# Optimization experiments

Hardware: AMD Instinct MI355X
Metric: run time of the kernel (lower is better)

## Reference

```python
import jax, jax.numpy as jnp
import numpy as np

K = 20
EPS_BN = 1e-5

def knn_idx(x, k):
    # x: [B,N,C] -> k nearest neighbor indices [B,N,k] (self included, as in DGCNN)
    sq = jnp.sum(x * x, axis=-1)                       # [B,N]
    inner = jnp.einsum('bnc,bmc->bnm', x, x)           # [B,N,N]
    neg_dist = 2.0 * inner - sq[:, :, None] - sq[:, None, :]
    _, idx = jax.lax.top_k(neg_dist, k)
    return jax.lax.stop_gradient(idx)

def edge_feat(x, idx):
    # x: [B,N,C], idx: [B,N,k] -> [B,N,k,2C] = cat([x_j - x_i, x_i])
    nbr = jax.vmap(lambda xb, ib: xb[ib])(x, idx)      # [B,N,k,C]
    ctr = jnp.broadcast_to(x[:, :, None, :], nbr.shape)
    return jnp.concatenate([nbr - ctr, ctr], axis=-1)

def edge_conv(x, W, g, b, k):
    e = edge_feat(x, knn_idx(x, k))                    # dynamic kNN graph per layer
    h = jnp.einsum('bnkc,cd->bnkd', e, W)              # 1x1 conv2d
    h = h * (g / jnp.sqrt(1.0 + EPS_BN)) + b           # BN eval (mean=0, var=1)
    return jnp.max(jax.nn.leaky_relu(h, 0.2), axis=2)  # max over neighbors -> [B,N,d]

def layer_norm(x, g, b):
    m = jnp.mean(x, axis=-1, keepdims=True)
    v = jnp.var(x, axis=-1, keepdims=True)
    return (x - m) * jax.lax.rsqrt(v + 1e-5) * g + b

def setup_inputs():
    key = jax.random.key(0)
    B, N = 2, 4096
    ks = jax.random.split(key, 16)
    w = lambda i, shape: jax.random.normal(ks[i], shape, jnp.float32) * 0.05
    ones = lambda d: jnp.ones((d,), jnp.float32)
    zeros = lambda d: jnp.zeros((d,), jnp.float32)
    return dict(
        xyz=jax.random.normal(ks[0], (N, 3), jnp.float32),
        scale=jax.random.normal(ks[1], (N, 3), jnp.float32),
        rot=jax.random.normal(ks[2], (N, 4), jnp.float32),
        opacity=jax.random.normal(ks[3], (N, 1), jnp.float32),
        color=jax.random.normal(ks[4], (N, 3), jnp.float32),
        pose=jax.random.normal(ks[5], (B, 75), jnp.float32),
        lbs_weights=jax.random.normal(ks[6], (N, 24), jnp.float32),
        Wc1=w(7, (226, 64)), g1=ones(64), b1=zeros(64),
        Wc2=w(8, (128, 64)), g2=ones(64), b2=zeros(64),
        Wc3=w(9, (128, 128)), g3=ones(128), b3=zeros(128),
        Wc4=w(10, (256, 256)), g4=ones(256), b4=zeros(256),
        Wc5=w(11, (512, 128)), g5=ones(128), b5=zeros(128),
        Wo1=w(12, (128, 128)), bo1=zeros(128), lg1=ones(128), lb1=zeros(128),
        Wo2=w(13, (128, 128)), bo2=zeros(128), lg2=ones(128), lb2=zeros(128),
        Wo3=w(14, (128, 38)), bo3=zeros(38),
    )

def reference(xyz, scale, rot, opacity, color, pose, lbs_weights,
              Wc1, g1, b1, Wc2, g2, b2, Wc3, g3, b3, Wc4, g4, b4, Wc5, g5, b5,
              Wo1, bo1, lg1, lb1, Wo2, bo2, lg2, lb2, Wo3, bo3):
    B, N = pose.shape[0], xyz.shape[0]
    gfeat = jnp.concatenate([xyz, scale, rot, opacity, color], axis=-1)   # [N,14]
    feats = jnp.concatenate([
        jnp.broadcast_to(gfeat[None], (B, N, gfeat.shape[-1])),
        jnp.broadcast_to(lbs_weights[None], (B, N, lbs_weights.shape[-1])),
        jnp.broadcast_to(pose[:, None, :], (B, N, pose.shape[-1])),
    ], axis=-1)                                                            # [B,N,113]
    # DGCNN graph encoder (dynamic kNN EdgeConv stack)
    x1 = edge_conv(feats, Wc1, g1, b1, K)   # [B,N,64]
    x2 = edge_conv(x1, Wc2, g2, b2, K)      # [B,N,64]
    x3 = edge_conv(x2, Wc3, g3, b3, K)      # [B,N,128]
    x4 = edge_conv(x3, Wc4, g4, b4, K)      # [B,N,256]
    cat = jnp.concatenate([x1, x2, x3, x4], axis=-1)                      # [B,N,512]
    gf = jax.nn.leaky_relu(
        jnp.einsum('bnc,cd->bnd', cat, Wc5) * (g5 / jnp.sqrt(1.0 + EPS_BN)) + b5, 0.2)
    # offset predictor MLP
    h = jax.nn.leaky_relu(layer_norm(gf @ Wo1 + bo1, lg1, lb1), 0.2)
    h = jax.nn.leaky_relu(layer_norm(h @ Wo2 + bo2, lg2, lb2), 0.2)
    off = h @ Wo3 + bo3                                                   # [B,N,38]
    # residual add of gaussian offsets (first 14 dims), lbs offsets raw (last 24)
    out = jnp.concatenate([gfeat[None] + off[..., :14], off[..., 14:]], axis=-1)
    return out                                                            # [B,N,38]
```

## Files before the change

kernel.cpp:

```cpp
#include <hip/hip_runtime.h>
#include <math.h>

#define KNN 20
#define BN_INV 0.9999950000374997f

__device__ __forceinline__ unsigned f2o(float f){
    unsigned u = __float_as_uint(f);
    return (u >> 31) ? ~u : (u | 0x80000000u);
}
__device__ __forceinline__ float o2f(unsigned u){
    return __uint_as_float((u >> 31) ? (u & 0x7fffffffu) : ~u);
}
__device__ __forceinline__ float leaky(float v){ return v > 0.f ? v : 0.2f * v; }

__global__ __launch_bounds__(128) void build_feats_kernel(
    const float* __restrict__ xyz, const float* __restrict__ scale,
    const float* __restrict__ rot, const float* __restrict__ opac,
    const float* __restrict__ color, const float* __restrict__ pose,
    const float* __restrict__ lbs, float* __restrict__ feats,
    float* __restrict__ sqout, int N)
{
    __shared__ float sred[2];
    int row = blockIdx.x;
    int b = row / N, n = row % N;
    int c = threadIdx.x;
    float v = 0.f;
    if      (c <   3) v = xyz  [n*3 + c];
    else if (c <   6) v = scale[n*3 + c-3];
    else if (c <  10) v = rot  [n*4 + c-6];
    else if (c <  11) v = opac [n];
    else if (c <  14) v = color[n*3 + c-11];
    else if (c <  38) v = lbs  [n*24 + c-14];
    else if (c < 113) v = pose [b*75 + c-38];
    if (c < 116) feats[(long)row*116 + c] = v;
    float ss = v * v;
    #pragma unroll
    for (int off = 32; off; off >>= 1) ss += __shfl_xor(ss, off);
    if ((c & 63) == 0) sred[c >> 6] = ss;
    __syncthreads();
    if (c == 0) sqout[row] = sred[0] + sred[1];
}


template<int C>
__global__ __launch_bounds__(256) void dist_gemm_kernel(
    const float* __restrict__ x, int N, int CP, float* __restrict__ G)
{
    __shared__ __align__(16) float smem[2*128*68];
    float (*xi)[68] = (float(*)[68])smem;
    float (*xj)[68] = (float(*)[68])(smem + 128*68);

    if (blockIdx.y < blockIdx.x) return;
    const int b  = blockIdx.z;
    const int bi = blockIdx.x * 128;
    const int bj = blockIdx.y * 128;
    const int t  = threadIdx.x;
    const int tx = t & 15, ty = t >> 4;
    const int CP4 = CP / 4;
    const long base = (long)b * N;
    const float4* xp = (const float4*)x;

    float acc[8][8] = {};

    for (int c0 = 0; c0 < C; c0 += 64){
        const int KCc = (C - c0 < 64) ? (C - c0) : 64;
        const int KC4 = KCc >> 2;
        __syncthreads();
        for (int f = t; f < 128 * KC4; f += 256){
            int r = f / KC4, c4 = f - r * KC4;
            float4 a = xp[(base + bi + r) * CP4 + (c0 >> 2) + c4];
            float4 bv = xp[(base + bj + r) * CP4 + (c0 >> 2) + c4];
            *(float4*)&xi[r][c4 * 4] = a;
            *(float4*)&xj[r][c4 * 4] = bv;
        }
        __syncthreads();
        for (int c = 0; c < KCc; c += 4){
            float4 A[8], Bv[8];
            #pragma unroll
            for (int ii = 0; ii < 8; ++ii) A[ii]  = *(const float4*)&xi[ty + 16*ii][c];
            #pragma unroll
            for (int jj = 0; jj < 8; ++jj) Bv[jj] = *(const float4*)&xj[tx + 16*jj][c];
            #pragma unroll
            for (int ii = 0; ii < 8; ++ii)
                #pragma unroll
                for (int jj = 0; jj < 8; ++jj){
                    acc[ii][jj] = fmaf(A[ii].x, Bv[jj].x, acc[ii][jj]);
                    acc[ii][jj] = fmaf(A[ii].y, Bv[jj].y, acc[ii][jj]);
                    acc[ii][jj] = fmaf(A[ii].z, Bv[jj].z, acc[ii][jj]);
                    acc[ii][jj] = fmaf(A[ii].w, Bv[jj].w, acc[ii][jj]);
                }
        }
    }

    #pragma unroll
    for (int ii = 0; ii < 8; ++ii){
        long rbase = (base + bi + ty + 16*ii) * N + bj;
        #pragma unroll
        for (int jj = 0; jj < 8; ++jj)
            G[rbase + tx + 16*jj] = acc[ii][jj];
    }

    if (bi != bj){
        __syncthreads();
        float (*tr)[132] = (float(*)[132])smem;
        #pragma unroll
        for (int ii = 0; ii < 8; ++ii)
            #pragma unroll
            for (int jj = 0; jj < 8; ++jj)
                tr[tx + 16*jj][ty + 16*ii] = acc[ii][jj];
        __syncthreads();
        const int r0 = t >> 5;
        const int cc = (t & 31) * 4;
        #pragma unroll
        for (int f = 0; f < 16; ++f){
            int r = r0 + 8 * f;
            *(float4*)&G[(base + bj + r) * N + bi + cc] = *(const float4*)&tr[r][cc];
        }
    }
}

#define TCAP 256
__global__ __launch_bounds__(256) void topk_kernel(
    const float* __restrict__ G, const float* __restrict__ sq,
    int N, int* __restrict__ idx_out)
{
    __shared__ unsigned smax[256];
    __shared__ unsigned cand_u[TCAP];
    __shared__ int      cand_j[TCAP];
    __shared__ unsigned cand_cnt;
    __shared__ unsigned sTu;

    const int row = blockIdx.x;
    const int b   = row >> 12;
    const int t   = threadIdx.x;
    const float4* g4  = (const float4*)(G  + (long)row * 4096);
    const float4* sq4 = (const float4*)(sq + (long)b   * 4096);

    unsigned u[16];
    #pragma unroll
    for (int qq = 0; qq < 4; ++qq){
        int v4 = t + 256 * qq;
        float4 gg = g4[v4];
        float4 ss = sq4[v4];
        u[4*qq+0] = f2o(fmaf(2.f, gg.x, -ss.x));
        u[4*qq+1] = f2o(fmaf(2.f, gg.y, -ss.y));
        u[4*qq+2] = f2o(fmaf(2.f, gg.z, -ss.z));
        u[4*qq+3] = f2o(fmaf(2.f, gg.w, -ss.w));
    }

    unsigned mu = u[0];
    #pragma unroll
    for (int q = 1; q < 16; ++q) mu = u[q] > mu ? u[q] : mu;
    smax[t] = mu;
    if (t == 0) cand_cnt = 0;
    __syncthreads();

    int rank = 0;
    for (int k = 0; k < 256; ++k){
        unsigned ou = smax[k];
        rank += (ou > mu) || (ou == mu && k < t);
    }
    if (rank == KNN - 1) sTu = mu;
    __syncthreads();
    const unsigned Tu = sTu;

    #pragma unroll
    for (int qq = 0; qq < 4; ++qq)
        #pragma unroll
        for (int m = 0; m < 4; ++m){
            int q = 4*qq + m;
            if (u[q] >= Tu){
                unsigned p = atomicAdd(&cand_cnt, 1u);
                if (p < TCAP){ cand_u[p] = u[q]; cand_j[p] = 4*(t + 256*qq) + m; }
            }
        }
    __syncthreads();
    const int cc = (int)cand_cnt;

    if (cc <= TCAP){
        if (t < cc){
            unsigned cu = cand_u[t]; int cj = cand_j[t];
            int r = 0;
            for (int k = 0; k < cc; ++k){
                unsigned ou = cand_u[k];
                r += (ou > cu) || (ou == cu && cand_j[k] < cj);
            }
            if (r < KNN) idx_out[(long)row * KNN + r] = cj;
        }
    } else {
        __shared__ unsigned rv[4]; __shared__ int ri[4]; __shared__ int gj_;
        unsigned lv = 0u; int lj = 0x7fffffff;
        #pragma unroll
        for (int q = 0; q < 16; ++q)
            if (u[q] > lv){ lv = u[q]; lj = 4*(t + 256*(q>>2)) + (q&3); }
        for (int it = 0; it < KNN; ++it){
            unsigned bv = lv; int bj = lj;
            #pragma unroll
            for (int off = 32; off; off >>= 1){
                unsigned ov = __shfl_xor(bv, off);
                int      oj = __shfl_xor(bj, off);
                if (ov > bv || (ov == bv && oj < bj)){ bv = ov; bj = oj; }
            }
            if ((t & 63) == 0){ rv[t >> 6] = bv; ri[t >> 6] = bj; }
            __syncthreads();
            if (t == 0){
                unsigned fv = rv[0]; int fj = ri[0];
                #pragma unroll
                for (int w = 1; w < 4; ++w)
                    if (rv[w] > fv || (rv[w] == fv && ri[w] < fj)){ fv = rv[w]; fj = ri[w]; }
                gj_ = fj;
                idx_out[(long)row * KNN + it] = fj;
            }
            __syncthreads();
            int fj = gj_;
            if (fj >= 0 && ((fj >> 2) & 255) == t){
                u[((fj >> 10) << 2) | (fj & 3)] = 0u;
                lv = 0u; lj = 0x7fffffff;
                #pragma unroll
                for (int q = 0; q < 16; ++q)
                    if (u[q] > lv){ lv = u[q]; lj = 4*(t + 256*(q>>2)) + (q&3); }
            }
            __syncthreads();
        }
    }
}


__global__ void prep_wcat_kernel(const float* __restrict__ W, int C, int CP, int D,
                                 float* __restrict__ Wcat)
{
    int i = blockIdx.x * 256 + threadIdx.x;
    int TWOD = 2 * D;
    if (i >= CP * TWOD) return;
    int c = i / TWOD, n = i - c * TWOD;
    float v = 0.f;
    if (c < C) v = (n < D) ? W[c*D + n] : (W[(C + c)*D + (n - D)] - W[c*D + (n - D)]);
    Wcat[i] = v;
}

__global__ __launch_bounds__(256) void gemm_pq_kernel(
    const float* __restrict__ X, int CP, const float* __restrict__ Wcat,
    const float* __restrict__ g, const float* __restrict__ bias,
    int D, int TWOD, float* __restrict__ PQ)
{
    __shared__ __align__(16) float As[128][68];
    __shared__ __align__(16) float Bs[64][132];
    const int bi = blockIdx.x * 128;
    const int bn = blockIdx.y * 128;
    const int t  = threadIdx.x;
    const int tx = t & 15, ty = t >> 4;
    const int CP4 = CP / 4;
    const float4* xp = (const float4*)X;

    float acc[8][8] = {};

    for (int c0 = 0; c0 < CP; c0 += 64){
        const int KC = (CP - c0 < 64) ? (CP - c0) : 64;
        const int KC4 = KC >> 2;
        __syncthreads();
        for (int f = t; f < 128 * KC4; f += 256){
            int r = f / KC4, c4 = f - r * KC4;
            *(float4*)&As[r][c4 * 4] = xp[(long)(bi + r) * CP4 + (c0 >> 2) + c4];
        }
        for (int f = t; f < KC * 32; f += 256){
            int r = f >> 5, c4 = f & 31;
            *(float4*)&Bs[r][c4 * 4] = *(const float4*)&Wcat[(long)(c0 + r) * TWOD + bn + c4 * 4];
        }
        __syncthreads();
        for (int c = 0; c < KC; c += 4){
            float4 A[8];
            #pragma unroll
            for (int ii = 0; ii < 8; ++ii) A[ii] = *(const float4*)&As[ty + 16*ii][c];
            float Bv0[8], Bv1[8], Bv2[8], Bv3[8];
            #pragma unroll
            for (int jj = 0; jj < 8; ++jj){
                Bv0[jj] = Bs[c+0][tx + 16*jj];
                Bv1[jj] = Bs[c+1][tx + 16*jj];
                Bv2[jj] = Bs[c+2][tx + 16*jj];
                Bv3[jj] = Bs[c+3][tx + 16*jj];
            }
            #pragma unroll
            for (int ii = 0; ii < 8; ++ii)
                #pragma unroll
                for (int jj = 0; jj < 8; ++jj){
                    acc[ii][jj] = fmaf(A[ii].x, Bv0[jj], acc[ii][jj]);
                    acc[ii][jj] = fmaf(A[ii].y, Bv1[jj], acc[ii][jj]);
                    acc[ii][jj] = fmaf(A[ii].z, Bv2[jj], acc[ii][jj]);
                    acc[ii][jj] = fmaf(A[ii].w, Bv3[jj], acc[ii][jj]);
                }
        }
    }

    #pragma unroll
    for (int jj = 0; jj < 8; ++jj){
        int n = bn + tx + 16*jj;
        int d = (n < D) ? n : n - D;
        float gg = g[d] * BN_INV;
        float bb = (n < D) ? 0.f : bias[d];
        #pragma unroll
        for (int ii = 0; ii < 8; ++ii)
            PQ[(long)(bi + ty + 16*ii) * TWOD + n] = fmaf(acc[ii][jj], gg, bb);
    }
}

template<int D, int RPB>
__global__ __launch_bounds__(256) void gather_max_kernel(
    const float* __restrict__ PQ, const int* __restrict__ idx, int N,
    float* __restrict__ y, float* __restrict__ sqout)
{
    __shared__ int   lidx[RPB][KNN];
    __shared__ float sred[4];
    const int rb = blockIdx.x * RPB;
    const int t  = threadIdx.x;
    if (t < RPB * KNN) lidx[t / KNN][t % KNN] = idx[(long)rb * KNN + t];
    __syncthreads();

    const int r = t / D, d = t - r * D;
    const int row = rb + r;
    const long base = (long)(row / N) * N;
    const int TWOD = 2 * D;

    float q = PQ[(long)row * TWOD + D + d];
    float m = -INFINITY;
    #pragma unroll
    for (int k = 0; k < KNN; ++k){
        int j = lidx[r][k];
        m = fmaxf(m, PQ[(base + j) * TWOD + d]);
    }
    float val = leaky(m + q);
    y[(long)row * D + d] = val;

    float ss = val * val;
    #pragma unroll
    for (int off = 32; off; off >>= 1) ss += __shfl_xor(ss, off);
    if ((t & 63) == 0) sred[t >> 6] = ss;
    __syncthreads();
    if (d == 0){
        constexpr int WPR = D / 64;
        float s = 0.f;
        int w0 = (r * D) >> 6;
        #pragma unroll
        for (int w = 0; w < WPR; ++w) s += sred[w0 + w];
        sqout[row] = s;
    }
}

__global__ __launch_bounds__(256) void knn_kernel(
    const float* __restrict__ x, int N, int CP4, int* __restrict__ idx_out)
{
    __shared__ float4 xi4[32];
    __shared__ float drow[4096];
    __shared__ float rv[4];
    __shared__ int   ri[4];

    int row = blockIdx.x;
    int b = row / N;
    int t = threadIdx.x;
    const float4* xp = (const float4*)x;

    if (t < CP4) xi4[t] = xp[(long)row * CP4 + t];
    __syncthreads();

    long bb = (long)b * N * CP4;
    for (int j = t; j < N; j += 256){
        const float4* p = xp + bb + (long)j * CP4;
        float acc = 0.f;
        #pragma unroll 4
        for (int c = 0; c < CP4; ++c){
            float4 xv = p[c], yv = xi4[c];
            float dx = xv.x - yv.x, dy = xv.y - yv.y;
            float dz = xv.z - yv.z, dw = xv.w - yv.w;
            acc += dx*dx + dy*dy + dz*dz + dw*dw;
        }
        drow[j] = -acc;
    }
    __syncthreads();

    for (int it = 0; it < KNN; ++it){
        float bv = -INFINITY; int bi = N;
        for (int j = t; j < N; j += 256){
            float v = drow[j];
            if (v > bv){ bv = v; bi = j; }
        }
        #pragma unroll
        for (int off = 32; off > 0; off >>= 1){
            float ov = __shfl_xor(bv, off);
            int   oi = __shfl_xor(bi, off);
            if (ov > bv || (ov == bv && oi < bi)){ bv = ov; bi = oi; }
        }
        if ((t & 63) == 0){ rv[t >> 6] = bv; ri[t >> 6] = bi; }
        __syncthreads();
        if (t == 0){
            float fv = rv[0]; int fi = ri[0];
            #pragma unroll
            for (int w = 1; w < 4; ++w){
                if (rv[w] > fv || (rv[w] == fv && ri[w] < fi)){ fv = rv[w]; fi = ri[w]; }
            }
            idx_out[(long)row * KNN + it] = fi;
            drow[fi] = -INFINITY;
        }
        __syncthreads();
    }
}

template<int D, int KPT>
__global__ __launch_bounds__(256) void edge_conv_kernel(
    const float* __restrict__ x, int N, int C, int CP,
    const float* __restrict__ W, const float* __restrict__ g,
    const float* __restrict__ bias, const int* __restrict__ idx,
    float* __restrict__ y, float* __restrict__ sqout)
{
    __shared__ float xi[128];
    __shared__ float nbr[KNN * 128];
    __shared__ float t2[D];
    __shared__ unsigned um[D];
    __shared__ float sred[4];

    int row = blockIdx.x;
    int b = row / N;
    int t = threadIdx.x;

    for (int c = t; c < C; c += 256) xi[c] = x[(long)row * CP + c];
    for (int kk = 0; kk < KNN; ++kk){
        int j = idx[(long)row * KNN + kk];
        long nb = ((long)b * N + j) * CP;
        for (int c = t; c < C; c += 256) nbr[kk * C + c] = x[nb + c];
    }
    __syncthreads();

    for (int d = t; d < D; d += 256){
        float s = 0.f;
        for (int c = 0; c < C; ++c) s += xi[c] * W[(C + c) * D + d];
        t2[d] = s; um[d] = 0u;
    }
    __syncthreads();

    const int d  = t % D;
    const int kg = t / D;
    float s[KPT];
    #pragma unroll
    for (int q = 0; q < KPT; ++q) s[q] = t2[d];

    const float* nb0 = &nbr[(kg * KPT) * C];
    for (int c = 0; c < C; ++c){
        float w   = W[c * D + d];
        float xic = xi[c];
        #pragma unroll
        for (int q = 0; q < KPT; ++q)
            s[q] += (nb0[q * C + c] - xic) * w;
    }
    float g_ = g[d] * BN_INV, b_ = bias[d];
    float m = -INFINITY;
    #pragma unroll
    for (int q = 0; q < KPT; ++q)
        m = fmaxf(m, leaky(s[q] * g_ + b_));
    atomicMax(&um[d], f2o(m));
    __syncthreads();

    float ss = 0.f;
    for (int dd = t; dd < D; dd += 256){
        float val = o2f(um[dd]);
        y[(long)row * D + dd] = val;
        ss += val * val;
    }
    #pragma unroll
    for (int off = 32; off; off >>= 1) ss += __shfl_xor(ss, off);
    if ((t & 63) == 0) sred[t >> 6] = ss;
    __syncthreads();
    if (t == 0) sqout[row] = sred[0] + sred[1] + sred[2] + sred[3];
}

#define HP 8
__global__ __launch_bounds__(128) void head_kernel(
    const float* __restrict__ x1, const float* __restrict__ x2,
    const float* __restrict__ x3, const float* __restrict__ x4,
    const float* __restrict__ feats,
    const float* __restrict__ Wc5, const float* __restrict__ g5, const float* __restrict__ b5,
    const float* __restrict__ Wo1, const float* __restrict__ bo1,
    const float* __restrict__ lg1, const float* __restrict__ lb1,
    const float* __restrict__ Wo2, const float* __restrict__ bo2,
    const float* __restrict__ lg2, const float* __restrict__ lb2,
    const float* __restrict__ Wo3, const float* __restrict__ bo3,
    float* __restrict__ out, int N, int R)
{
    __shared__ __align__(16) float cat[HP][520];
    __shared__ __align__(16) float hb[HP][132];
    __shared__ float wsum[2][HP], wsq[2][HP];
    __shared__ float f14[HP][14];

    const int t = threadIdx.x;
    const long p0 = (long)blockIdx.x * HP;
    const int wid = t >> 6;

    long rows[HP];
    #pragma unroll
    for (int p = 0; p < HP; ++p){
        long row = p0 + p; if (row >= R) row = R - 1;
        rows[p] = row;
        cat[p][t]       = (t < 64) ? x1[row*64 + t] : x2[row*64 + (t-64)];
        cat[p][128 + t] = x3[row*128 + t];
        cat[p][256 + t] = x4[row*256 + t];
        cat[p][384 + t] = x4[row*256 + 128 + t];
        if (t < 14) f14[p][t] = feats[row*116 + t];
    }
    __syncthreads();

    const float g5t = g5[t] * BN_INV, b5t = b5[t];
    float acc[HP];
    #pragma unroll
    for (int p = 0; p < HP; ++p) acc[p] = 0.f;
    for (int c4 = 0; c4 < 128; ++c4){
        float w0 = Wc5[(4*c4+0)*128 + t];
        float w1 = Wc5[(4*c4+1)*128 + t];
        float w2 = Wc5[(4*c4+2)*128 + t];
        float w3 = Wc5[(4*c4+3)*128 + t];
        #pragma unroll
        for (int p = 0; p < HP; ++p){
            float4 cv = *(const float4*)&cat[p][4*c4];
            acc[p] = fmaf(cv.x, w0, acc[p]);
            acc[p] = fmaf(cv.y, w1, acc[p]);
            acc[p] = fmaf(cv.z, w2, acc[p]);
            acc[p] = fmaf(cv.w, w3, acc[p]);
        }
    }
    #pragma unroll
    for (int p = 0; p < HP; ++p) hb[p][t] = leaky(fmaf(acc[p], g5t, b5t));
    __syncthreads();

    for (int layer = 0; layer < 2; ++layer){
        const float* W  = layer ? Wo2 : Wo1;
        const float* bo = layer ? bo2 : bo1;
        const float* lg = layer ? lg2 : lg1;
        const float* lb = layer ? lb2 : lb1;
        float a2[HP];
        float bot = bo[t];
        #pragma unroll
        for (int p = 0; p < HP; ++p) a2[p] = bot;
        for (int c4 = 0; c4 < 32; ++c4){
            float w0 = W[(4*c4+0)*128 + t];
            float w1 = W[(4*c4+1)*128 + t];
            float w2 = W[(4*c4+2)*128 + t];
            float w3 = W[(4*c4+3)*128 + t];
            #pragma unroll
            for (int p = 0; p < HP; ++p){
                float4 hv = *(const float4*)&hb[p][4*c4];
                a2[p] = fmaf(hv.x, w0, a2[p]);
                a2[p] = fmaf(hv.y, w1, a2[p]);
                a2[p] = fmaf(hv.z, w2, a2[p]);
                a2[p] = fmaf(hv.w, w3, a2[p]);
            }
        }
        #pragma unroll
        for (int p = 0; p < HP; ++p){
            float s1 = a2[p], s2 = a2[p]*a2[p];
            #pragma unroll
            for (int off = 32; off; off >>= 1){
                s1 += __shfl_xor(s1, off);
                s2 += __shfl_xor(s2, off);
            }
            if ((t & 63) == 0){ wsum[wid][p] = s1; wsq[wid][p] = s2; }
        }
        __syncthreads();
        float lgt = lg[t], lbt = lb[t];
        float hn[HP];
        #pragma unroll
        for (int p = 0; p < HP; ++p){
            float m  = (wsum[0][p] + wsum[1][p]) * (1.f/128.f);
            float v  = (wsq[0][p]  + wsq[1][p])  * (1.f/128.f) - m*m;
            float dm = a2[p] - m;
            hn[p] = leaky(dm * rsqrtf(v + 1e-5f) * lgt + lbt);
        }
        __syncthreads();
        #pragma unroll
        for (int p = 0; p < HP; ++p) hb[p][t] = hn[p];
        __syncthreads();
    }

    if (t < 38){
        float o[HP];
        float bt = bo3[t];
        #pragma unroll
        for (int p = 0; p < HP; ++p) o[p] = bt;
        for (int c = 0; c < 128; ++c){
            float w = Wo3[c*38 + t];
            #pragma unroll
            for (int p = 0; p < HP; ++p) o[p] = fmaf(hb[p][c], w, o[p]);
        }
        #pragma unroll
        for (int p = 0; p < HP; ++p){
            float val = o[p] + ((t < 14) ? f14[p][t] : 0.f);
            out[rows[p]*38 + t] = val;
        }
    }
}

extern "C" void kernel_launch(void* const* d_in, const int* in_sizes, int n_in,
                              void* d_out, int out_size, void* d_ws, size_t ws_size,
                              hipStream_t stream)
{
    const float* xyz  = (const float*)d_in[0];
    const float* scal = (const float*)d_in[1];
    const float* rot  = (const float*)d_in[2];
    const float* opac = (const float*)d_in[3];
    const float* colr = (const float*)d_in[4];
    const float* pose = (const float*)d_in[5];
    const float* lbs  = (const float*)d_in[6];
    const float* Wc1 = (const float*)d_in[7];  const float* g1 = (const float*)d_in[8];  const float* b1 = (const float*)d_in[9];
    const float* Wc2 = (const float*)d_in[10]; const float* g2 = (const float*)d_in[11]; const float* b2 = (const float*)d_in[12];
    const float* Wc3 = (const float*)d_in[13]; const float* g3 = (const float*)d_in[14]; const float* b3 = (const float*)d_in[15];
    const float* Wc4 = (const float*)d_in[16]; const float* g4 = (const float*)d_in[17]; const float* b4 = (const float*)d_in[18];
    const float* Wc5 = (const float*)d_in[19]; const float* g5 = (const float*)d_in[20]; const float* b5 = (const float*)d_in[21];
    const float* Wo1 = (const float*)d_in[22]; const float* bo1 = (const float*)d_in[23];
    const float* lg1 = (const float*)d_in[24]; const float* lb1 = (const float*)d_in[25];
    const float* Wo2 = (const float*)d_in[26]; const float* bo2 = (const float*)d_in[27];
    const float* lg2 = (const float*)d_in[28]; const float* lb2 = (const float*)d_in[29];
    const float* Wo3 = (const float*)d_in[30]; const float* bo3 = (const float*)d_in[31];

    const int N = in_sizes[0] / 3;
    const int B = in_sizes[5] / 75;
    const int R = B * N;

    char* ws = (char*)d_ws;
    size_t o = 0;
    float* feats = (float*)(ws + o); o += (size_t)R * 116 * 4;
    float* x1    = (float*)(ws + o); o += (size_t)R * 64  * 4;
    float* x2    = (float*)(ws + o); o += (size_t)R * 64  * 4;
    float* x3    = (float*)(ws + o); o += (size_t)R * 128 * 4;
    float* x4    = (float*)(ws + o); o += (size_t)R * 256 * 4;
    int*   idx   = (int*)  (ws + o); o += (size_t)R * KNN * 4;
    float* sq    = (float*)(ws + o); o += (size_t)R * 4;
    float* Wcat  = (float*)(ws + o); o += (size_t)128 * 512 * 4;
    float* G     = (float*)(ws + o);
    float* PQ    = G;
    size_t need  = o + (size_t)B * N * N * 4;

    const bool fast = (N == 4096) && (ws_size >= need);

    build_feats_kernel<<<R, 128, 0, stream>>>(xyz, scal, rot, opac, colr, pose, lbs, feats, sq, N);

    if (fast){
        dim3 gg(N/128, N/128, B);

        dist_gemm_kernel<116><<<gg, 256, 0, stream>>>(feats, N, 116, G);
        topk_kernel<<<R, 256, 0, stream>>>(G, sq, N, idx);
        prep_wcat_kernel<<<(116*128 + 255)/256, 256, 0, stream>>>(Wc1, 113, 116, 64, Wcat);
        gemm_pq_kernel<<<dim3(R/128, 1), 256, 0, stream>>>(feats, 116, Wcat, g1, b1, 64, 128, PQ);
        gather_max_kernel<64, 4><<<R/4, 256, 0, stream>>>(PQ, idx, N, x1, sq);

        dist_gemm_kernel<64><<<gg, 256, 0, stream>>>(x1, N, 64, G);
        topk_kernel<<<R, 256, 0, stream>>>(G, sq, N, idx);
        prep_wcat_kernel<<<(64*128 + 255)/256, 256, 0, stream>>>(Wc2, 64, 64, 64, Wcat);
        gemm_pq_kernel<<<dim3(R/128, 1), 256, 0, stream>>>(x1, 64, Wcat, g2, b2, 64, 128, PQ);
        gather_max_kernel<64, 4><<<R/4, 256, 0, stream>>>(PQ, idx, N, x2, sq);

        dist_gemm_kernel<64><<<gg, 256, 0, stream>>>(x2, N, 64, G);
        topk_kernel<<<R, 256, 0, stream>>>(G, sq, N, idx);
        prep_wcat_kernel<<<(64*256 + 255)/256, 256, 0, stream>>>(Wc3, 64, 64, 128, Wcat);
        gemm_pq_kernel<<<dim3(R/128, 2), 256, 0, stream>>>(x2, 64, Wcat, g3, b3, 128, 256, PQ);
        gather_max_kernel<128, 2><<<R/2, 256, 0, stream>>>(PQ, idx, N, x3, sq);

        dist_gemm_kernel<128><<<gg, 256, 0, stream>>>(x3, N, 128, G);
        topk_kernel<<<R, 256, 0, stream>>>(G, sq, N, idx);
        prep_wcat_kernel<<<(128*512 + 255)/256, 256, 0, stream>>>(Wc4, 128, 128, 256, Wcat);
        gemm_pq_kernel<<<dim3(R/128, 4), 256, 0, stream>>>(x3, 128, Wcat, g4, b4, 256, 512, PQ);
        gather_max_kernel<256, 1><<<R, 256, 0, stream>>>(PQ, idx, N, x4, sq);
    } else {
        knn_kernel<<<R, 256, 0, stream>>>(feats, N, 116/4, idx);
        edge_conv_kernel<64, 5><<<R, 256, 0, stream>>>(feats, N, 113, 116, Wc1, g1, b1, idx, x1, sq);
        knn_kernel<<<R, 256, 0, stream>>>(x1, N, 64/4, idx);
        edge_conv_kernel<64, 5><<<R, 256, 0, stream>>>(x1, N, 64, 64, Wc2, g2, b2, idx, x2, sq);
        knn_kernel<<<R, 256, 0, stream>>>(x2, N, 64/4, idx);
        edge_conv_kernel<128, 10><<<R, 256, 0, stream>>>(x2, N, 64, 64, Wc3, g3, b3, idx, x3, sq);
        knn_kernel<<<R, 256, 0, stream>>>(x3, N, 128/4, idx);
        edge_conv_kernel<256, 20><<<R, 256, 0, stream>>>(x3, N, 128, 128, Wc4, g4, b4, idx, x4, sq);
    }

    head_kernel<<<(R + HP - 1)/HP, 128, 0, stream>>>(x1, x2, x3, x4, feats,
                                       Wc5, g5, b5, Wo1, bo1, lg1, lb1,
                                       Wo2, bo2, lg2, lb2, Wo3, bo3,
                                       (float*)d_out, N, R);
}
```

Baseline: 936.2 us.

## Shrink dist-GEMM smem, launch only upper-triangle tiles, batch weight prep

The distance GEMM now stages 32-channel K slices, cutting shared memory from about 68KB to 36KB. It also writes the transposed tile in two halves, which should let more blocks sit on each CU. The grid enumerates only upper-triangular tile pairs, decoding the pair index with a sqrt instead of launching and early-exiting lower-triangle blocks. The four per-layer weight-concat prep kernels are merged into one launch at the start, with a larger Wcat buffer. The cost is more K-loop iterations and barriers per tile, plus a small index-decode overhead.

After: 842.3 us. 1.11x faster.

```diff
diff --git a/kernel.cpp b/kernel.cpp
--- a/kernel.cpp
+++ b/kernel.cpp
@@ -46,14 +46,19 @@
 __global__ __launch_bounds__(256) void dist_gemm_kernel(
     const float* __restrict__ x, int N, int CP, float* __restrict__ G)
 {
-    __shared__ __align__(16) float smem[2*128*68];
-    float (*xi)[68] = (float(*)[68])smem;
-    float (*xj)[68] = (float(*)[68])(smem + 128*68);
-
-    if (blockIdx.y < blockIdx.x) return;
+    __shared__ __align__(16) float smem[9216];
+    float (*xi)[36] = (float(*)[36])smem;
+    float (*xj)[36] = (float(*)[36])(smem + 128*36);
+
+    const int q = blockIdx.x;
+    int bjt = (int)((sqrtf(8.f*(float)q + 1.f) - 1.f) * 0.5f);
+    while ((bjt+1)*(bjt+2)/2 <= q) ++bjt;
+    while (bjt*(bjt+1)/2 > q) --bjt;
+    const int bit = q - bjt*(bjt+1)/2;
+    const int bi = bit * 128;
+    const int bj = bjt * 128;
+
     const int b  = blockIdx.z;
-    const int bi = blockIdx.x * 128;
-    const int bj = blockIdx.y * 128;
     const int t  = threadIdx.x;
     const int tx = t & 15, ty = t >> 4;
     const int CP4 = CP / 4;
@@ -62,19 +67,25 @@
 
     float acc[8][8] = {};
 
-    for (int c0 = 0; c0 < C; c0 += 64){
-        const int KCc = (C - c0 < 64) ? (C - c0) : 64;
-        const int KC4 = KCc >> 2;
-        __syncthreads();
-        for (int f = t; f < 128 * KC4; f += 256){
-            int r = f / KC4, c4 = f - r * KC4;
-            float4 a = xp[(base + bi + r) * CP4 + (c0 >> 2) + c4];
-            float4 bv = xp[(base + bj + r) * CP4 + (c0 >> 2) + c4];
-            *(float4*)&xi[r][c4 * 4] = a;
-            *(float4*)&xj[r][c4 * 4] = bv;
-        }
-        __syncthreads();
-        for (int c = 0; c < KCc; c += 4){
+    for (int c0 = 0; c0 < C; c0 += 32){
+        const int KC  = (C - c0 < 32) ? (C - c0) : 32;
+        const int KC4 = KC >> 2;
+        __syncthreads();
+        if (KC4 == 8){
+            for (int f = t; f < 128 * 8; f += 256){
+                int r = f >> 3, c4 = f & 7;
+                *(float4*)&xi[r][c4 * 4] = xp[(base + bi + r) * CP4 + (c0 >> 2) + c4];
+                *(float4*)&xj[r][c4 * 4] = xp[(base + bj + r) * CP4 + (c0 >> 2) + c4];
+            }
+        } else {
+            for (int f = t; f < 128 * KC4; f += 256){
+                int r = f / KC4, c4 = f - r * KC4;
+                *(float4*)&xi[r][c4 * 4] = xp[(base + bi + r) * CP4 + (c0 >> 2) + c4];
+                *(float4*)&xj[r][c4 * 4] = xp[(base + bj + r) * CP4 + (c0 >> 2) + c4];
+            }
+        }
+        __syncthreads();
+        for (int c = 0; c < KC; c += 4){
             float4 A[8], Bv[8];
             #pragma unroll
             for (int ii = 0; ii < 8; ++ii) A[ii]  = *(const float4*)&xi[ty + 16*ii][c];
@@ -101,20 +112,23 @@
     }
 
     if (bi != bj){
-        __syncthreads();
         float (*tr)[132] = (float(*)[132])smem;
         #pragma unroll
-        for (int ii = 0; ii < 8; ++ii)
-            #pragma unroll
-            for (int jj = 0; jj < 8; ++jj)
-                tr[tx + 16*jj][ty + 16*ii] = acc[ii][jj];
-        __syncthreads();
-        const int r0 = t >> 5;
-        const int cc = (t & 31) * 4;
-        #pragma unroll
-        for (int f = 0; f < 16; ++f){
-            int r = r0 + 8 * f;
-            *(float4*)&G[(base + bj + r) * N + bi + cc] = *(const float4*)&tr[r][cc];
+        for (int h = 0; h < 2; ++h){
+            __syncthreads();
+            #pragma unroll
+            for (int ii = 0; ii < 8; ++ii)
+                #pragma unroll
+                for (int jj = 4*h; jj < 4*h + 4; ++jj)
+                    tr[tx + 16*(jj - 4*h)][ty + 16*ii] = acc[ii][jj];
+            __syncthreads();
+            const int cc = (t & 31) * 4;
+            const int r0 = t >> 5;
+            #pragma unroll
+            for (int f = 0; f < 8; ++f){
+                int r = r0 + 8 * f;
+                *(float4*)&G[(base + bj + 64*h + r) * N + bi + cc] = *(const float4*)&tr[r][cc];
+            }
         }
     }
 }
@@ -226,16 +240,26 @@
 }
 
 
-__global__ void prep_wcat_kernel(const float* __restrict__ W, int C, int CP, int D,
-                                 float* __restrict__ Wcat)
-{
-    int i = blockIdx.x * 256 + threadIdx.x;
+__device__ __forceinline__ void wcat_emit(const float* __restrict__ W, int C, int D,
+                                          int i, float* __restrict__ dst)
+{
     int TWOD = 2 * D;
-    if (i >= CP * TWOD) return;
     int c = i / TWOD, n = i - c * TWOD;
     float v = 0.f;
     if (c < C) v = (n < D) ? W[c*D + n] : (W[(C + c)*D + (n - D)] - W[c*D + (n - D)]);
-    Wcat[i] = v;
+    dst[i] = v;
+}
+
+__global__ void prep_all_wcat_kernel(
+    const float* __restrict__ Wc1, const float* __restrict__ Wc2,
+    const float* __restrict__ Wc3, const float* __restrict__ Wc4,
+    float* __restrict__ Wcat)
+{
+    int i = blockIdx.x * 256 + threadIdx.x;
+    if      (i <  14848) wcat_emit(Wc1, 113,  64, i,          Wcat);
+    else if (i <  23040) wcat_emit(Wc2,  64,  64, i - 14848,  Wcat + 14848);
+    else if (i <  39424) wcat_emit(Wc3,  64, 128, i - 23040,  Wcat + 23040);
+    else if (i < 104960) wcat_emit(Wc4, 128, 256, i - 39424,  Wcat + 39424);
 }
 
 __global__ __launch_bounds__(256) void gemm_pq_kernel(
@@ -629,7 +653,7 @@
     float* x4    = (float*)(ws + o); o += (size_t)R * 256 * 4;
     int*   idx   = (int*)  (ws + o); o += (size_t)R * KNN * 4;
     float* sq    = (float*)(ws + o); o += (size_t)R * 4;
-    float* Wcat  = (float*)(ws + o); o += (size_t)128 * 512 * 4;
+    float* Wcat  = (float*)(ws + o); o += (size_t)104960 * 4;
     float* G     = (float*)(ws + o);
     float* PQ    = G;
     size_t need  = o + (size_t)B * N * N * 4;
@@ -639,30 +663,33 @@
     build_feats_kernel<<<R, 128, 0, stream>>>(xyz, scal, rot, opac, colr, pose, lbs, feats, sq, N);
 
     if (fast){
-        dim3 gg(N/128, N/128, B);
+        const int NT = 32;
+        dim3 gg(NT*(NT+1)/2, 1, B);
+        float* Wcat1 = Wcat;
+        float* Wcat2 = Wcat + 14848;
+        float* Wcat3 = Wcat + 23040;
+        float* Wcat4 = Wcat + 39424;
+
+        prep_all_wcat_kernel<<<(104960 + 255)/256, 256, 0, stream>>>(Wc1, Wc2, Wc3, Wc4, Wcat);
 
         dist_gemm_kernel<116><<<gg, 256, 0, stream>>>(feats, N, 116, G);
         topk_kernel<<<R, 256, 0, stream>>>(G, sq, N, idx);
-        prep_wcat_kernel<<<(116*128 + 255)/256, 256, 0, stream>>>(Wc1, 113, 116, 64, Wcat);
-        gemm_pq_kernel<<<dim3(R/128, 1), 256, 0, stream>>>(feats, 116, Wcat, g1, b1, 64, 128, PQ);
+        gemm_pq_kernel<<<dim3(R/128, 1), 256, 0, stream>>>(feats, 116, Wcat1, g1, b1, 64, 128, PQ);
         gather_max_kernel<64, 4><<<R/4, 256, 0, stream>>>(PQ, idx, N, x1, sq);
 
         dist_gemm_kernel<64><<<gg, 256, 0, stream>>>(x1, N, 64, G);
         topk_kernel<<<R, 256, 0, stream>>>(G, sq, N, idx);
-        prep_wcat_kernel<<<(64*128 + 255)/256, 256, 0, stream>>>(Wc2, 64, 64, 64, Wcat);
-        gemm_pq_kernel<<<dim3(R/128, 1), 256, 0, stream>>>(x1, 64, Wcat, g2, b2, 64, 128, PQ);
+        gemm_pq_kernel<<<dim3(R/128, 1), 256, 0, stream>>>(x1, 64, Wcat2, g2, b2, 64, 128, PQ);
         gather_max_kernel<64, 4><<<R/4, 256, 0, stream>>>(PQ, idx, N, x2, sq);
 
         dist_gemm_kernel<64><<<gg, 256, 0, stream>>>(x2, N, 64, G);
         topk_kernel<<<R, 256, 0, stream>>>(G, sq, N, idx);
-        prep_wcat_kernel<<<(64*256 + 255)/256, 256, 0, stream>>>(Wc3, 64, 64, 128, Wcat);
-        gemm_pq_kernel<<<dim3(R/128, 2), 256, 0, stream>>>(x2, 64, Wcat, g3, b3, 128, 256, PQ);
+        gemm_pq_kernel<<<dim3(R/128, 2), 256, 0, stream>>>(x2, 64, Wcat3, g3, b3, 128, 256, PQ);
         gather_max_kernel<128, 2><<<R/2, 256, 0, stream>>>(PQ, idx, N, x3, sq);
 
         dist_gemm_kernel<128><<<gg, 256, 0, stream>>>(x3, N, 128, G);
         topk_kernel<<<R, 256, 0, stream>>>(G, sq, N, idx);
-        prep_wcat_kernel<<<(128*512 + 255)/256, 256, 0, stream>>>(Wc4, 128, 128, 256, Wcat);
-        gemm_pq_kernel<<<dim3(R/128, 4), 256, 0, stream>>>(x3, 128, Wcat, g4, b4, 256, 512, PQ);
+        gemm_pq_kernel<<<dim3(R/128, 4), 256, 0, stream>>>(x3, 128, Wcat4, g4, b4, 256, 512, PQ);
         gather_max_kernel<256, 1><<<R, 256, 0, stream>>>(PQ, idx, N, x4, sq);
     } else {
         knn_kernel<<<R, 256, 0, stream>>>(feats, N, 116/4, idx);
```
